# Kernel optimization log

Hardware: AMD Instinct MI355X
Metric: run time of the kernel (lower is better)

The kernel has to match this reference:

```python
import jax, jax.numpy as jnp
import numpy as np

TOP_K = 2


def setup_inputs() -> dict:
    key = jax.random.key(0)
    k_x, k_g, k_w1, k_w2, k_w3 = jax.random.split(key, 5)
    B, S, D, H, E = 2, 512, 1024, 512, 8
    x = jax.random.normal(k_x, (B, S, D), dtype=jnp.float32)
    gate_w = jax.random.normal(k_g, (D, E), dtype=jnp.float32) * (D ** -0.5)
    w1 = jax.random.normal(k_w1, (E, D, H), dtype=jnp.float32) * 0.02  # gate proj
    w2 = jax.random.normal(k_w2, (E, H, D), dtype=jnp.float32) * 0.02  # down proj
    w3 = jax.random.normal(k_w3, (E, D, H), dtype=jnp.float32) * 0.02  # up proj
    return {"x": x, "gate_w": gate_w, "w1": w1, "w2": w2, "w3": w3}


def reference(x, gate_w, w1, w2, w3):
    # Token-choice top-k MoE with grouped SwiGLU experts, no shared expert.
    # Equivalent to torchtune MoE: gather routed tokens, scale by top-k router
    # score, run per-expert FFN, scatter-add back. Since each expert's FFN has
    # no bias (FFN(0) == 0), the dispatch/grouped-GEMM/combine is expressed
    # densely as sum_e FFN_e(scale[:, e] * x), which is mathematically identical.
    B, S, D = x.shape
    E = gate_w.shape[1]
    xf = x.reshape(B * S, D)                      # [T, D]
    T = B * S

    logits = xf @ gate_w                          # [T, E]
    scores = jax.nn.softmax(logits, axis=-1)
    top_scores, top_idx = jax.lax.top_k(scores, TOP_K)  # [T, k]

    # scale[t, e] = router score if expert e selected for token t, else 0
    scale = jnp.zeros((T, E), dtype=x.dtype).at[
        jnp.arange(T)[:, None], top_idx
    ].set(top_scores)

    xs = scale.T[:, :, None] * xf[None, :, :]     # [E, T, D] scaled routed input
    h = jax.nn.silu(jnp.einsum('etd,edh->eth', xs, w1)) \
        * jnp.einsum('etd,edh->eth', xs, w3)      # [E, T, H]
    y = jnp.einsum('eth,ehd->etd', h, w2)         # [E, T, D]
    out = y.sum(axis=0)                           # combine (scatter-add equiv)
    return out.reshape(B, S, D)
```

## Files before the change

kernel.cpp:

```cpp
#include <hip/hip_runtime.h>
#include <hip/hip_bf16.h>
#include <cstddef>

#define T_TOK 1024
#define D_DIM 1024
#define H_DIM 512
#define E_EXP 8
#define P_CAP 2560
#define MAX_MT 40
#define LDA 72
#define NK1 16
#define NK2 8

typedef __attribute__((ext_vector_type(4)))  float    float4_t;
typedef __attribute__((ext_vector_type(16))) float    f32x16;
typedef __attribute__((ext_vector_type(8)))  short    short8_t;
typedef __attribute__((ext_vector_type(4)))  unsigned uint4_t;

__device__ __forceinline__ short f2bf(float f) {
  union { float f; unsigned u; } v; v.f = f;
  unsigned u = v.u;
  u += 0x7FFFu + ((u >> 16) & 1u);
  return (short)(u >> 16);
}

__device__ __forceinline__ unsigned pkbf(float a, float b) {
  union { __hip_bfloat162 h; unsigned u; } v;
  v.h = __float22bfloat162_rn(make_float2(a, b));
  return v.u;
}

__global__ __launch_bounds__(256) void prep_kernel(
    const float* __restrict__ w1, const float* __restrict__ w3,
    const float* __restrict__ w2, const float* __restrict__ x,
    const float* __restrict__ gw, short* __restrict__ w13t,
    short* __restrict__ w2t, int* __restrict__ idx2,
    float* __restrict__ scale2, float* __restrict__ out) {
  __shared__ float tile[64][69];
  const int u = blockIdx.x;
  const int tid = threadIdx.x;

  if (u < 3072) {
    const float* src; short* dst; int N, ldd, row_off, k0, n0;
    if (u < 2048) {
      int z = u >> 7, rem = u & 127;
      int kt = rem & 15, nt = rem >> 4;
      int which = z >> 3, e = z & 7;
      src = (which ? w3 : w1) + (size_t)e * D_DIM * H_DIM;
      dst = w13t + (size_t)e * D_DIM * (2 * H_DIM);
      N = H_DIM; ldd = D_DIM; row_off = which ? H_DIM : 0;
      k0 = kt * 64; n0 = nt * 64;
    } else {
      int v = u - 2048;
      int e = v >> 7, rem = v & 127;
      int kt = rem & 7, nt = rem >> 3;
      src = w2 + (size_t)e * H_DIM * D_DIM;
      dst = w2t + (size_t)e * D_DIM * H_DIM;
      N = D_DIM; ldd = H_DIM; row_off = 0;
      k0 = kt * 64; n0 = nt * 64;
    }
    const int kr = tid >> 4, nc = (tid & 15) * 4;
    #pragma unroll
    for (int p = 0; p < 4; ++p) {
      int k = p * 16 + kr;
      float4_t v = *(const float4_t*)(src + (size_t)(k0 + k) * N + n0 + nc);
      tile[k][nc]     = v[0];
      tile[k][nc + 1] = v[1];
      tile[k][nc + 2] = v[2];
      tile[k][nc + 3] = v[3];
    }
    __syncthreads();
    const int r8 = tid >> 3, c8 = tid & 7;
    #pragma unroll
    for (int p = 0; p < 2; ++p) {
      int row = p * 32 + r8;
      uint4_t uu;
      #pragma unroll
      for (int jj = 0; jj < 4; ++jj)
        uu[jj] = pkbf(tile[c8 * 8 + 2 * jj][row], tile[c8 * 8 + 2 * jj + 1][row]);
      *(uint4_t*)(dst + (size_t)(row_off + n0 + row) * ldd + k0 + c8 * 8) = uu;
    }
    return;
  }

  if (u >= 3328) {
    int v = u - 3328;
    float4_t z4 = {0.f, 0.f, 0.f, 0.f};
    float4_t* o = (float4_t*)(out + (size_t)v * 4096);
    #pragma unroll
    for (int i = 0; i < 4; ++i) o[i * 256 + tid] = z4;
    return;
  }

  const int wid  = tid >> 6;
  const int lane = tid & 63;
  const int t = (u - 3072) * 4 + wid;
  const float* xr = x + (size_t)t * D_DIM;
  float acc[E_EXP];
  #pragma unroll
  for (int e = 0; e < E_EXP; ++e) acc[e] = 0.f;
  for (int d = lane; d < D_DIM; d += 64) {
    float xv = xr[d];
    float4_t g0 = *(const float4_t*)(gw + d * E_EXP);
    float4_t g1 = *(const float4_t*)(gw + d * E_EXP + 4);
    acc[0] += xv * g0[0]; acc[1] += xv * g0[1];
    acc[2] += xv * g0[2]; acc[3] += xv * g0[3];
    acc[4] += xv * g1[0]; acc[5] += xv * g1[1];
    acc[6] += xv * g1[2]; acc[7] += xv * g1[3];
  }
  #pragma unroll
  for (int off = 32; off >= 1; off >>= 1) {
    #pragma unroll
    for (int e = 0; e < E_EXP; ++e) acc[e] += __shfl_down(acc[e], off, 64);
  }
  if (lane == 0) {
    float m = acc[0];
    #pragma unroll
    for (int e = 1; e < E_EXP; ++e) m = fmaxf(m, acc[e]);
    float p[E_EXP]; float s = 0.f;
    #pragma unroll
    for (int e = 0; e < E_EXP; ++e) { p[e] = __expf(acc[e] - m); s += p[e]; }
    float inv = 1.f / s;
    #pragma unroll
    for (int e = 0; e < E_EXP; ++e) p[e] *= inv;
    int i1 = 0;
    #pragma unroll
    for (int e = 1; e < E_EXP; ++e) if (p[e] > p[i1]) i1 = e;
    int i2 = (i1 == 0) ? 1 : 0;
    #pragma unroll
    for (int e = 0; e < E_EXP; ++e) {
      if (e == i1 || e == i2) continue;
      if (p[e] > p[i2]) i2 = e;
    }
    idx2[2 * t]     = i1;  scale2[2 * t]     = p[i1];
    idx2[2 * t + 1] = i2;  scale2[2 * t + 1] = p[i2];
  }
}

__global__ __launch_bounds__(256) void scan_kernel(
    const int* __restrict__ idx2, const float* __restrict__ scale2,
    int* __restrict__ pair_tok, float* __restrict__ pair_scale,
    int* __restrict__ meta) {
  __shared__ int wcnt[16][E_EXP];
  __shared__ int woff[16][E_EXP];
  __shared__ int sbase[E_EXP], stot[E_EXP];
  const int tid = threadIdx.x;
  const int lane = tid & 63, wv = tid >> 6;
  const unsigned long long lt = (1ull << lane) - 1ull;

  for (int p = tid; p < P_CAP; p += 256) { pair_tok[p] = -1; pair_scale[p] = 0.f; }

  int e0[4], e1[4];
  #pragma unroll
  for (int c = 0; c < 4; ++c) {
    int t = c * 256 + wv * 64 + lane;
    e0[c] = idx2[2 * t];
    e1[c] = idx2[2 * t + 1];
  }
  #pragma unroll
  for (int c = 0; c < 4; ++c) {
    #pragma unroll
    for (int e = 0; e < E_EXP; ++e) {
      unsigned long long m0 = __ballot(e0[c] == e);
      unsigned long long m1 = __ballot(e1[c] == e);
      if (lane == 0) wcnt[c * 4 + wv][e] = __popcll(m0) + __popcll(m1);
    }
  }
  __syncthreads();
  if (tid < E_EXP) {
    int s = 0;
    for (int r = 0; r < 16; ++r) s += wcnt[r][tid];
    stot[tid] = s;
  }
  __syncthreads();
  if (tid == 0) {
    int b = 0, g = 0;
    for (int e = 0; e < E_EXP; ++e) {
      sbase[e] = b;
      int al = (stot[e] + 63) & ~63;
      for (int j = 0; j < al; j += 64) { meta[1 + g] = e; meta[81 + g] = b + j; ++g; }
      b += al;
    }
    meta[0] = g;
  }
  __syncthreads();
  if (tid < E_EXP) {
    int run = sbase[tid];
    for (int r = 0; r < 16; ++r) { woff[r][tid] = run; run += wcnt[r][tid]; }
  }
  __syncthreads();
  #pragma unroll
  for (int c = 0; c < 4; ++c) {
    int t = c * 256 + wv * 64 + lane;
    int a0 = e0[c], a1 = e1[c];
    #pragma unroll
    for (int e = 0; e < E_EXP; ++e) {
      unsigned long long m0 = __ballot(a0 == e);
      unsigned long long m1 = __ballot(a1 == e);
      int base = woff[c * 4 + wv][e];
      if (a0 == e) {
        int pos = base + (int)__popcll(m0 & lt);
        pair_tok[pos] = t; pair_scale[pos] = scale2[2 * t];
      }
      if (a1 == e) {
        int pos = base + (int)__popcll(m0) + (int)__popcll(m1 & lt);
        pair_tok[pos] = t; pair_scale[pos] = scale2[2 * t + 1];
      }
    }
  }
}

__global__ __launch_bounds__(256, 2) void gemm1_kernel(
    const float* __restrict__ x, const short* __restrict__ w13t,
    const int* __restrict__ pair_tok, const float* __restrict__ pair_scale,
    const int* __restrict__ meta, short* __restrict__ h) {
  __shared__ short As[2][64 * LDA];
  __shared__ short B1s[2][64 * LDA];
  __shared__ short B3s[2][64 * LDA];
  const int mt = blockIdx.y;
  if (mt >= meta[0]) return;
  const int e    = meta[1 + mt];
  const int row0 = meta[81 + mt];
  const int n0   = blockIdx.x * 64;
  const int tid = threadIdx.x, lane = tid & 63, wid = tid >> 6;
  const int wm = wid >> 1, wn = wid & 1;
  const int l31 = lane & 31, lh = lane >> 5;
  const short* bsrc = w13t + (size_t)e * D_DIM * (2 * H_DIM);

  const int sr = tid >> 3, su = (tid & 7) * 8;
  const size_t st32 = (size_t)32 * D_DIM;
  const int   tok0 = pair_tok[row0 + sr];
  const int   tok1 = pair_tok[row0 + sr + 32];
  const float sc0  = pair_scale[row0 + sr];
  const float sc1  = pair_scale[row0 + sr + 32];
  const float* xr0 = x + (size_t)(tok0 < 0 ? 0 : tok0) * D_DIM + su;
  const float* xr1 = x + (size_t)(tok1 < 0 ? 0 : tok1) * D_DIM + su;
  const short* ap1 = bsrc + (size_t)(n0 + sr) * D_DIM + su;
  const short* ap3 = bsrc + (size_t)(H_DIM + n0 + sr) * D_DIM + su;

  f32x16 acc1, acc3;
  #pragma unroll
  for (int i = 0; i < 16; ++i) { acc1[i] = 0.f; acc3[i] = 0.f; }

  {
    float4_t v0 = *(const float4_t*)(xr0);
    float4_t v1 = *(const float4_t*)(xr0 + 4);
    float4_t w0 = *(const float4_t*)(xr1);
    float4_t w1v = *(const float4_t*)(xr1 + 4);
    uint4_t a0 = {pkbf(v0[0] * sc0, v0[1] * sc0), pkbf(v0[2] * sc0, v0[3] * sc0),
                  pkbf(v1[0] * sc0, v1[1] * sc0), pkbf(v1[2] * sc0, v1[3] * sc0)};
    uint4_t a1 = {pkbf(w0[0] * sc1, w0[1] * sc1), pkbf(w0[2] * sc1, w0[3] * sc1),
                  pkbf(w1v[0] * sc1, w1v[1] * sc1), pkbf(w1v[2] * sc1, w1v[3] * sc1)};
    uint4_t p0 = *(const uint4_t*)ap1;
    uint4_t p1 = *(const uint4_t*)(ap1 + st32);
    uint4_t q0 = *(const uint4_t*)ap3;
    uint4_t q1 = *(const uint4_t*)(ap3 + st32);
    *(uint4_t*)&As[0][sr * LDA + su]         = a0;
    *(uint4_t*)&As[0][(sr + 32) * LDA + su]  = a1;
    *(uint4_t*)&B1s[0][sr * LDA + su]        = p0;
    *(uint4_t*)&B1s[0][(sr + 32) * LDA + su] = p1;
    *(uint4_t*)&B3s[0][sr * LDA + su]        = q0;
    *(uint4_t*)&B3s[0][(sr + 32) * LDA + su] = q1;
  }

  for (int t = 0; t < NK1 - 1; ++t) {
    __syncthreads();
    const int cur = t & 1, nxt = cur ^ 1;
    const int ko = (t + 1) * 64;
    float4_t v0 = *(const float4_t*)(xr0 + ko);
    float4_t v1 = *(const float4_t*)(xr0 + ko + 4);
    float4_t w0 = *(const float4_t*)(xr1 + ko);
    float4_t w1v = *(const float4_t*)(xr1 + ko + 4);
    uint4_t p0 = *(const uint4_t*)(ap1 + ko);
    uint4_t p1 = *(const uint4_t*)(ap1 + st32 + ko);
    uint4_t q0 = *(const uint4_t*)(ap3 + ko);
    uint4_t q1 = *(const uint4_t*)(ap3 + st32 + ko);

    short8_t af[4], b1f[4], b3f[4];
    #pragma unroll
    for (int s = 0; s < 4; ++s) {
      const int kof = s * 16 + lh * 8;
      af[s]  = *(const short8_t*)&As[cur][(wm * 32 + l31) * LDA + kof];
      b1f[s] = *(const short8_t*)&B1s[cur][(wn * 32 + l31) * LDA + kof];
      b3f[s] = *(const short8_t*)&B3s[cur][(wn * 32 + l31) * LDA + kof];
    }
    #pragma unroll
    for (int s = 0; s < 4; ++s) {
      acc1 = __builtin_amdgcn_mfma_f32_32x32x16_bf16(af[s], b1f[s], acc1, 0, 0, 0);
      acc3 = __builtin_amdgcn_mfma_f32_32x32x16_bf16(af[s], b3f[s], acc3, 0, 0, 0);
    }
    uint4_t a0 = {pkbf(v0[0] * sc0, v0[1] * sc0), pkbf(v0[2] * sc0, v0[3] * sc0),
                  pkbf(v1[0] * sc0, v1[1] * sc0), pkbf(v1[2] * sc0, v1[3] * sc0)};
    uint4_t a1 = {pkbf(w0[0] * sc1, w0[1] * sc1), pkbf(w0[2] * sc1, w0[3] * sc1),
                  pkbf(w1v[0] * sc1, w1v[1] * sc1), pkbf(w1v[2] * sc1, w1v[3] * sc1)};
    *(uint4_t*)&As[nxt][sr * LDA + su]         = a0;
    *(uint4_t*)&As[nxt][(sr + 32) * LDA + su]  = a1;
    *(uint4_t*)&B1s[nxt][sr * LDA + su]        = p0;
    *(uint4_t*)&B1s[nxt][(sr + 32) * LDA + su] = p1;
    *(uint4_t*)&B3s[nxt][sr * LDA + su]        = q0;
    *(uint4_t*)&B3s[nxt][(sr + 32) * LDA + su] = q1;
  }
  __syncthreads();
  {
    short8_t af[4], b1f[4], b3f[4];
    #pragma unroll
    for (int s = 0; s < 4; ++s) {
      const int kof = s * 16 + lh * 8;
      af[s]  = *(const short8_t*)&As[1][(wm * 32 + l31) * LDA + kof];
      b1f[s] = *(const short8_t*)&B1s[1][(wn * 32 + l31) * LDA + kof];
      b3f[s] = *(const short8_t*)&B3s[1][(wn * 32 + l31) * LDA + kof];
    }
    #pragma unroll
    for (int s = 0; s < 4; ++s) {
      acc1 = __builtin_amdgcn_mfma_f32_32x32x16_bf16(af[s], b1f[s], acc1, 0, 0, 0);
      acc3 = __builtin_amdgcn_mfma_f32_32x32x16_bf16(af[s], b3f[s], acc3, 0, 0, 0);
    }
  }

  {
    const int col = n0 + wn * 32 + l31;
    #pragma unroll
    for (int r = 0; r < 16; ++r) {
      int mrow = (r & 3) + 8 * (r >> 2) + 4 * lh;
      int grow = row0 + wm * 32 + mrow;
      float c1 = acc1[r], c3 = acc3[r];
      float sig = 1.f / (1.f + __expf(-c1));
      h[(size_t)grow * H_DIM + col] = f2bf(c1 * sig * c3);
    }
  }
}

__global__ __launch_bounds__(256, 2) void gemm2_kernel(
    const short* __restrict__ h, const short* __restrict__ w2t,
    const int* __restrict__ pair_tok, const int* __restrict__ meta,
    float* __restrict__ out) {
  __shared__ short As[2][64 * LDA];
  __shared__ short Bs[2][128 * LDA];
  const int mt = blockIdx.y;
  if (mt >= meta[0]) return;
  const int e    = meta[1 + mt];
  const int row0 = meta[81 + mt];
  const int n0   = blockIdx.x * 128;
  const int tid = threadIdx.x, lane = tid & 63, wid = tid >> 6;
  const int wm = wid >> 1, wn = wid & 1;
  const int l31 = lane & 31, lh = lane >> 5;
  const short* bsrc = w2t + (size_t)e * D_DIM * H_DIM;

  const int sr = tid >> 3, su = (tid & 7) * 8;
  const size_t st32 = (size_t)32 * H_DIM;
  const short* apA = h    + (size_t)(row0 + sr) * H_DIM + su;
  const short* apB = bsrc + (size_t)(n0 + sr) * H_DIM + su;

  f32x16 accA, accB;
  #pragma unroll
  for (int i = 0; i < 16; ++i) { accA[i] = 0.f; accB[i] = 0.f; }

  {
    uint4_t a0 = *(const uint4_t*)apA;
    uint4_t a1 = *(const uint4_t*)(apA + st32);
    uint4_t b0 = *(const uint4_t*)apB;
    uint4_t b1 = *(const uint4_t*)(apB + st32);
    uint4_t b2 = *(const uint4_t*)(apB + 2 * st32);
    uint4_t b3 = *(const uint4_t*)(apB + 3 * st32);
    *(uint4_t*)&As[0][sr * LDA + su]        = a0;
    *(uint4_t*)&As[0][(sr + 32) * LDA + su] = a1;
    *(uint4_t*)&Bs[0][sr * LDA + su]        = b0;
    *(uint4_t*)&Bs[0][(sr + 32) * LDA + su] = b1;
    *(uint4_t*)&Bs[0][(sr + 64) * LDA + su] = b2;
    *(uint4_t*)&Bs[0][(sr + 96) * LDA + su] = b3;
  }

  for (int t = 0; t < NK2 - 1; ++t) {
    __syncthreads();
    const int cur = t & 1, nxt = cur ^ 1;
    const int ko = (t + 1) * 64;
    uint4_t a0 = *(const uint4_t*)(apA + ko);
    uint4_t a1 = *(const uint4_t*)(apA + st32 + ko);
    uint4_t b0 = *(const uint4_t*)(apB + ko);
    uint4_t b1 = *(const uint4_t*)(apB + st32 + ko);
    uint4_t b2 = *(const uint4_t*)(apB + 2 * st32 + ko);
    uint4_t b3 = *(const uint4_t*)(apB + 3 * st32 + ko);

    short8_t af[4], bf0[4], bf1[4];
    #pragma unroll
    for (int s = 0; s < 4; ++s) {
      const int kof = s * 16 + lh * 8;
      af[s]  = *(const short8_t*)&As[cur][(wm * 32 + l31) * LDA + kof];
      bf0[s] = *(const short8_t*)&Bs[cur][(wn * 64 + l31) * LDA + kof];
      bf1[s] = *(const short8_t*)&Bs[cur][(wn * 64 + 32 + l31) * LDA + kof];
    }
    #pragma unroll
    for (int s = 0; s < 4; ++s) {
      accA = __builtin_amdgcn_mfma_f32_32x32x16_bf16(af[s], bf0[s], accA, 0, 0, 0);
      accB = __builtin_amdgcn_mfma_f32_32x32x16_bf16(af[s], bf1[s], accB, 0, 0, 0);
    }
    *(uint4_t*)&As[nxt][sr * LDA + su]        = a0;
    *(uint4_t*)&As[nxt][(sr + 32) * LDA + su] = a1;
    *(uint4_t*)&Bs[nxt][sr * LDA + su]        = b0;
    *(uint4_t*)&Bs[nxt][(sr + 32) * LDA + su] = b1;
    *(uint4_t*)&Bs[nxt][(sr + 64) * LDA + su] = b2;
    *(uint4_t*)&Bs[nxt][(sr + 96) * LDA + su] = b3;
  }
  __syncthreads();
  {
    short8_t af[4], bf0[4], bf1[4];
    #pragma unroll
    for (int s = 0; s < 4; ++s) {
      const int kof = s * 16 + lh * 8;
      af[s]  = *(const short8_t*)&As[1][(wm * 32 + l31) * LDA + kof];
      bf0[s] = *(const short8_t*)&Bs[1][(wn * 64 + l31) * LDA + kof];
      bf1[s] = *(const short8_t*)&Bs[1][(wn * 64 + 32 + l31) * LDA + kof];
    }
    #pragma unroll
    for (int s = 0; s < 4; ++s) {
      accA = __builtin_amdgcn_mfma_f32_32x32x16_bf16(af[s], bf0[s], accA, 0, 0, 0);
      accB = __builtin_amdgcn_mfma_f32_32x32x16_bf16(af[s], bf1[s], accB, 0, 0, 0);
    }
  }

  {
    #pragma unroll
    for (int r = 0; r < 16; ++r) {
      int mrow = (r & 3) + 8 * (r >> 2) + 4 * lh;
      int grow = row0 + wm * 32 + mrow;
      int tok = pair_tok[grow];
      if (tok < 0) continue;
      float* orow = out + (size_t)tok * D_DIM;
      atomicAdd(orow + n0 + wn * 64 + l31, accA[r]);
      atomicAdd(orow + n0 + wn * 64 + 32 + l31, accB[r]);
    }
  }
}

extern "C" void kernel_launch(void* const* d_in, const int* in_sizes, int n_in,
                              void* d_out, int out_size, void* d_ws, size_t ws_size,
                              hipStream_t stream) {
  const float* x  = (const float*)d_in[0];
  const float* gw = (const float*)d_in[1];
  const float* w1 = (const float*)d_in[2];
  const float* w2 = (const float*)d_in[3];
  const float* w3 = (const float*)d_in[4];
  float* out = (float*)d_out;

  char* ws = (char*)d_ws;
  int*   idx2    = (int*)  (ws);
  float* scale2  = (float*)(ws + 8192);
  int*   ptok    = (int*)  (ws + 16384);
  float* pscale  = (float*)(ws + 32768);
  int*   meta    = (int*)  (ws + 49152);
  short* h       = (short*)(ws + (1u << 20));
  short* w13t    = (short*)(ws + (4u << 20));
  short* w2t     = (short*)(ws + (21u << 20));

  prep_kernel<<<dim3(3584), dim3(256), 0, stream>>>(
      w1, w3, w2, x, gw, w13t, w2t, idx2, scale2, out);
  scan_kernel<<<dim3(1), dim3(256), 0, stream>>>(idx2, scale2, ptok, pscale, meta);
  gemm1_kernel<<<dim3(H_DIM / 64, MAX_MT), dim3(256), 0, stream>>>(
      x, w13t, ptok, pscale, meta, h);
  gemm2_kernel<<<dim3(D_DIM / 128, MAX_MT), dim3(256), 0, stream>>>(
      h, w2t, ptok, meta, out);
}
```

Baseline: 152.7 us.

## Fuse routing scan into GEMM kernels, recomputing per-block token lists

Removes the single-block scan kernel and its launch. Each GEMM block now recomputes expert counts, prefix offsets and its own 64-row slice of routed tokens in shared memory, reading straight from idx2/scale2. This drops one serialized launch and the global pair/meta arrays. In exchange, every block of both GEMMs repeats the ballot-based counting over all 2048 pairs and uses extra shared memory, which could lower occupancy.

```diff
diff --git a/kernel.cpp b/kernel.cpp
--- a/kernel.cpp
+++ b/kernel.cpp
@@ -6,7 +6,6 @@
 #define D_DIM 1024
 #define H_DIM 512
 #define E_EXP 8
-#define P_CAP 2560
 #define MAX_MT 40
 #define LDA 72
 #define NK1 16
@@ -137,102 +136,98 @@
   }
 }
 
-__global__ __launch_bounds__(256) void scan_kernel(
+__device__ __forceinline__ bool route_block(
     const int* __restrict__ idx2, const float* __restrict__ scale2,
-    int* __restrict__ pair_tok, float* __restrict__ pair_scale,
-    int* __restrict__ meta) {
-  __shared__ int wcnt[16][E_EXP];
-  __shared__ int woff[16][E_EXP];
-  __shared__ int sbase[E_EXP], stot[E_EXP];
-  const int tid = threadIdx.x;
-  const int lane = tid & 63, wv = tid >> 6;
+    int mt, int tid, int (&wcnt)[32][E_EXP], int (&woff)[32][E_EXP],
+    int (&scnt)[E_EXP], int (&ltok)[64], float (&lsc)[64],
+    int& e_sel, int& grow0) {
+  const int lane = tid & 63, wv4 = tid >> 6;
   const unsigned long long lt = (1ull << lane) - 1ull;
 
-  for (int p = tid; p < P_CAP; p += 256) { pair_tok[p] = -1; pair_scale[p] = 0.f; }
-
-  int e0[4], e1[4];
-  #pragma unroll
-  for (int c = 0; c < 4; ++c) {
-    int t = c * 256 + wv * 64 + lane;
-    e0[c] = idx2[2 * t];
-    e1[c] = idx2[2 * t + 1];
-  }
-  #pragma unroll
-  for (int c = 0; c < 4; ++c) {
+  int ex[8];
+  #pragma unroll
+  for (int c = 0; c < 8; ++c) ex[c] = idx2[c * 256 + wv4 * 64 + lane];
+
+  #pragma unroll
+  for (int c = 0; c < 8; ++c) {
     #pragma unroll
     for (int e = 0; e < E_EXP; ++e) {
-      unsigned long long m0 = __ballot(e0[c] == e);
-      unsigned long long m1 = __ballot(e1[c] == e);
-      if (lane == 0) wcnt[c * 4 + wv][e] = __popcll(m0) + __popcll(m1);
-    }
-  }
+      unsigned long long m = __ballot(ex[c] == e);
+      if (lane == 0) wcnt[c * 4 + wv4][e] = (int)__popcll(m);
+    }
+  }
+  if (tid < 64) { ltok[tid] = -1; lsc[tid] = 0.f; }
   __syncthreads();
-  if (tid < E_EXP) {
-    int s = 0;
-    for (int r = 0; r < 16; ++r) s += wcnt[r][tid];
-    stot[tid] = s;
+  {
+    int g = tid >> 3, e = tid & 7;
+    int pre = 0;
+    for (int gg = 0; gg < g; ++gg) pre += wcnt[gg][e];
+    woff[g][e] = pre;
+    if (g == 31) scnt[e] = pre + wcnt[31][e];
   }
   __syncthreads();
-  if (tid == 0) {
-    int b = 0, g = 0;
+  int row0 = -1;
+  {
+    int accT = 0, base = 0;
+    e_sel = -1; grow0 = -1;
+    #pragma unroll
     for (int e = 0; e < E_EXP; ++e) {
-      sbase[e] = b;
-      int al = (stot[e] + 63) & ~63;
-      for (int j = 0; j < al; j += 64) { meta[1 + g] = e; meta[81 + g] = b + j; ++g; }
-      b += al;
-    }
-    meta[0] = g;
+      int ce = scnt[e];
+      int nt = (ce + 63) >> 6;
+      if (mt >= accT && mt < accT + nt) {
+        e_sel = e; row0 = (mt - accT) * 64; grow0 = base + row0;
+      }
+      accT += nt; base += nt * 64;
+    }
+    if (mt >= accT) return false;
+  }
+  #pragma unroll
+  for (int c = 0; c < 8; ++c) {
+    int p = c * 256 + wv4 * 64 + lane;
+    int myE = ex[c];
+    unsigned long long msel = 0;
+    #pragma unroll
+    for (int e = 0; e < E_EXP; ++e) {
+      unsigned long long m = __ballot(myE == e);
+      if (myE == e) msel = m;
+    }
+    int r = woff[c * 4 + wv4][myE] + (int)__popcll(msel & lt);
+    if (myE == e_sel && r >= row0 && r < row0 + 64) {
+      ltok[r - row0] = p >> 1;
+      lsc[r - row0]  = scale2[p];
+    }
   }
   __syncthreads();
-  if (tid < E_EXP) {
-    int run = sbase[tid];
-    for (int r = 0; r < 16; ++r) { woff[r][tid] = run; run += wcnt[r][tid]; }
-  }
-  __syncthreads();
-  #pragma unroll
-  for (int c = 0; c < 4; ++c) {
-    int t = c * 256 + wv * 64 + lane;
-    int a0 = e0[c], a1 = e1[c];
-    #pragma unroll
-    for (int e = 0; e < E_EXP; ++e) {
-      unsigned long long m0 = __ballot(a0 == e);
-      unsigned long long m1 = __ballot(a1 == e);
-      int base = woff[c * 4 + wv][e];
-      if (a0 == e) {
-        int pos = base + (int)__popcll(m0 & lt);
-        pair_tok[pos] = t; pair_scale[pos] = scale2[2 * t];
-      }
-      if (a1 == e) {
-        int pos = base + (int)__popcll(m0) + (int)__popcll(m1 & lt);
-        pair_tok[pos] = t; pair_scale[pos] = scale2[2 * t + 1];
-      }
-    }
-  }
+  return true;
 }
 
 __global__ __launch_bounds__(256, 2) void gemm1_kernel(
     const float* __restrict__ x, const short* __restrict__ w13t,
-    const int* __restrict__ pair_tok, const float* __restrict__ pair_scale,
-    const int* __restrict__ meta, short* __restrict__ h) {
+    const int* __restrict__ idx2, const float* __restrict__ scale2,
+    short* __restrict__ h) {
   __shared__ short As[2][64 * LDA];
   __shared__ short B1s[2][64 * LDA];
   __shared__ short B3s[2][64 * LDA];
+  __shared__ int wcnt[32][E_EXP], woff[32][E_EXP], scnt[E_EXP], ltok[64];
+  __shared__ float lsc[64];
   const int mt = blockIdx.y;
-  if (mt >= meta[0]) return;
-  const int e    = meta[1 + mt];
-  const int row0 = meta[81 + mt];
+  const int tid = threadIdx.x, lane = tid & 63, wid = tid >> 6;
+
+  int e_sel, grow0;
+  if (!route_block(idx2, scale2, mt, tid, wcnt, woff, scnt, ltok, lsc,
+                   e_sel, grow0)) return;
+
   const int n0   = blockIdx.x * 64;
-  const int tid = threadIdx.x, lane = tid & 63, wid = tid >> 6;
   const int wm = wid >> 1, wn = wid & 1;
   const int l31 = lane & 31, lh = lane >> 5;
-  const short* bsrc = w13t + (size_t)e * D_DIM * (2 * H_DIM);
+  const short* bsrc = w13t + (size_t)e_sel * D_DIM * (2 * H_DIM);
 
   const int sr = tid >> 3, su = (tid & 7) * 8;
   const size_t st32 = (size_t)32 * D_DIM;
-  const int   tok0 = pair_tok[row0 + sr];
-  const int   tok1 = pair_tok[row0 + sr + 32];
-  const float sc0  = pair_scale[row0 + sr];
-  const float sc1  = pair_scale[row0 + sr + 32];
+  const int   tok0 = ltok[sr];
+  const int   tok1 = ltok[sr + 32];
+  const float sc0  = lsc[sr];
+  const float sc1  = lsc[sr + 32];
   const float* xr0 = x + (size_t)(tok0 < 0 ? 0 : tok0) * D_DIM + su;
   const float* xr1 = x + (size_t)(tok1 < 0 ? 0 : tok1) * D_DIM + su;
   const short* ap1 = bsrc + (size_t)(n0 + sr) * D_DIM + su;
@@ -322,7 +317,7 @@
     #pragma unroll
     for (int r = 0; r < 16; ++r) {
       int mrow = (r & 3) + 8 * (r >> 2) + 4 * lh;
-      int grow = row0 + wm * 32 + mrow;
+      int grow = grow0 + wm * 32 + mrow;
       float c1 = acc1[r], c3 = acc3[r];
       float sig = 1.f / (1.f + __expf(-c1));
       h[(size_t)grow * H_DIM + col] = f2bf(c1 * sig * c3);
@@ -332,23 +327,27 @@
 
 __global__ __launch_bounds__(256, 2) void gemm2_kernel(
     const short* __restrict__ h, const short* __restrict__ w2t,
-    const int* __restrict__ pair_tok, const int* __restrict__ meta,
+    const int* __restrict__ idx2, const float* __restrict__ scale2,
     float* __restrict__ out) {
   __shared__ short As[2][64 * LDA];
   __shared__ short Bs[2][128 * LDA];
+  __shared__ int wcnt[32][E_EXP], woff[32][E_EXP], scnt[E_EXP], ltok[64];
+  __shared__ float lsc[64];
   const int mt = blockIdx.y;
-  if (mt >= meta[0]) return;
-  const int e    = meta[1 + mt];
-  const int row0 = meta[81 + mt];
+  const int tid = threadIdx.x, lane = tid & 63, wid = tid >> 6;
+
+  int e_sel, grow0;
+  if (!route_block(idx2, scale2, mt, tid, wcnt, woff, scnt, ltok, lsc,
+                   e_sel, grow0)) return;
+
   const int n0   = blockIdx.x * 128;
-  const int tid = threadIdx.x, lane = tid & 63, wid = tid >> 6;
   const int wm = wid >> 1, wn = wid & 1;
   const int l31 = lane & 31, lh = lane >> 5;
-  const short* bsrc = w2t + (size_t)e * D_DIM * H_DIM;
+  const short* bsrc = w2t + (size_t)e_sel * D_DIM * H_DIM;
 
   const int sr = tid >> 3, su = (tid & 7) * 8;
   const size_t st32 = (size_t)32 * H_DIM;
-  const short* apA = h    + (size_t)(row0 + sr) * H_DIM + su;
+  const short* apA = h    + (size_t)(grow0 + sr) * H_DIM + su;
   const short* apB = bsrc + (size_t)(n0 + sr) * H_DIM + su;
 
   f32x16 accA, accB;
@@ -422,8 +421,7 @@
     #pragma unroll
     for (int r = 0; r < 16; ++r) {
       int mrow = (r & 3) + 8 * (r >> 2) + 4 * lh;
-      int grow = row0 + wm * 32 + mrow;
-      int tok = pair_tok[grow];
+      int tok = ltok[wm * 32 + mrow];
       if (tok < 0) continue;
       float* orow = out + (size_t)tok * D_DIM;
       atomicAdd(orow + n0 + wn * 64 + l31, accA[r]);
@@ -445,18 +443,14 @@
   char* ws = (char*)d_ws;
   int*   idx2    = (int*)  (ws);
   float* scale2  = (float*)(ws + 8192);
-  int*   ptok    = (int*)  (ws + 16384);
-  float* pscale  = (float*)(ws + 32768);
-  int*   meta    = (int*)  (ws + 49152);
   short* h       = (short*)(ws + (1u << 20));
   short* w13t    = (short*)(ws + (4u << 20));
   short* w2t     = (short*)(ws + (21u << 20));
 
   prep_kernel<<<dim3(3584), dim3(256), 0, stream>>>(
       w1, w3, w2, x, gw, w13t, w2t, idx2, scale2, out);
-  scan_kernel<<<dim3(1), dim3(256), 0, stream>>>(idx2, scale2, ptok, pscale, meta);
   gemm1_kernel<<<dim3(H_DIM / 64, MAX_MT), dim3(256), 0, stream>>>(
-      x, w13t, ptok, pscale, meta, h);
+      x, w13t, idx2, scale2, h);
   gemm2_kernel<<<dim3(D_DIM / 128, MAX_MT), dim3(256), 0, stream>>>(
-      h, w2t, ptok, meta, out);
-}
+      h, w2t, idx2, scale2, out);
+}
```

New measurement: 147.7 us. 3.3% less time.
